# Optimization experiments

Measured on AMD Instinct MI355X. Metric: run time of the kernel, lower is better.

Reference implementation:

```python
import jax, jax.numpy as jnp
import numpy as np

N_NODES = 50000
N_EDGES = 800000
F_IN = 128
HEADS = 4
OUT_C = 32
NEG_SLOPE = 0.2


def setup_inputs() -> dict:
    key = jax.random.key(0)
    ks = jax.random.split(key, 6)
    x = jax.random.normal(ks[0], (N_NODES, F_IN), dtype=jnp.float32)
    edge_index = jax.random.randint(ks[1], (2, N_EDGES), 0, N_NODES, dtype=jnp.int32)
    scale = 1.0 / np.sqrt(F_IN)
    W_l = jax.random.normal(ks[2], (F_IN, HEADS * OUT_C), dtype=jnp.float32) * scale
    W_r = jax.random.normal(ks[3], (F_IN, HEADS * OUT_C), dtype=jnp.float32) * scale
    b_l = jnp.zeros((HEADS * OUT_C,), dtype=jnp.float32)
    b_r = jnp.zeros((HEADS * OUT_C,), dtype=jnp.float32)
    att = jax.random.normal(ks[4], (1, HEADS, OUT_C), dtype=jnp.float32) * (1.0 / np.sqrt(OUT_C))
    bias = jnp.zeros((HEADS * OUT_C,), dtype=jnp.float32)
    return {"x": x, "edge_index": edge_index, "W_l": W_l, "b_l": b_l,
            "W_r": W_r, "b_r": b_r, "att": att, "bias": bias}


def reference(x, edge_index, W_l, b_l, W_r, b_r, att, bias):
    N = x.shape[0]
    H, C = HEADS, OUT_C
    src, dst = edge_index[0], edge_index[1]  # messages flow src(j) -> dst(i)

    x_l = (x @ W_l + b_l).reshape(N, H, C)  # Theta_t x (source/message transform)
    x_r = (x @ W_r + b_r).reshape(N, H, C)  # Theta_s x (target transform)

    # per-edge GATv2 score: a^T LeakyReLU(x_l[j] + x_r[i])
    e = x_l[src] + x_r[dst]                        # [E, H, C]
    e = jnp.where(e > 0, e, NEG_SLOPE * e)         # LeakyReLU
    alpha = jnp.sum(e * att, axis=-1)              # [E, H]

    # segment softmax over incoming edges of each dst node
    amax = jax.ops.segment_max(alpha, dst, num_segments=N)   # [N, H]
    amax = jnp.where(jnp.isfinite(amax), amax, 0.0)
    expa = jnp.exp(alpha - amax[dst])                        # [E, H]
    denom = jax.ops.segment_sum(expa, dst, num_segments=N)   # [N, H]
    alpha = expa / (denom[dst] + 1e-16)                      # [E, H]

    # scatter-aggregate messages: sum_j alpha_ij * x_l[j]
    msg = alpha[:, :, None] * x_l[src]                       # [E, H, C]
    out = jax.ops.segment_sum(msg, dst, num_segments=N)      # [N, H, C]
    out = out.reshape(N, H * C) + bias                       # concat heads + bias
    return out
```

## Files before the change

kernel.cpp:

```cpp
#include <hip/hip_runtime.h>
#include <math.h>

#define NNODES 50000
#define NEDGES 800000
#define FIN 128
#define HC 128
#define NHEADS 4
#define NEG 0.2f
#define CAP 64
#define RANGE ((NNODES + 7) / 8)
#define GEMMB (((NNODES + 63) / 64) * 2)
#define HCHUNK ((NEDGES + 2047) / 2048)
#define HISTB (HCHUNK * 8)
#define ZB    ((NNODES + 255) / 256)
#define WTB   128

typedef _Float16 half8 __attribute__((ext_vector_type(8)));
typedef _Float16 half4v __attribute__((ext_vector_type(4)));
typedef float    f32x4 __attribute__((ext_vector_type(4)));

__global__ __launch_bounds__(256) void zero_wt_kernel(int* __restrict__ deg,
                                                      const float* __restrict__ Wl,
                                                      const float* __restrict__ Wr,
                                                      _Float16* __restrict__ Wt) {
    int t = threadIdx.x;
    if (blockIdx.x < ZB) {
        int i = blockIdx.x * 256 + t;
        if (i < NNODES) deg[i] = 0;
        return;
    }
    int flat = (blockIdx.x - ZB) * 256 + t;
    int k = flat >> 8, c = flat & 255;
    float v = (c < 128) ? Wl[(size_t)k * 128 + c] : Wr[(size_t)k * 128 + (c - 128)];
    Wt[(size_t)c * 128 + k] = (_Float16)v;
}

__global__ __launch_bounds__(256) void gemm_kernel(const float* __restrict__ x,
                                                   const _Float16* __restrict__ Wt,
                                                   const float* __restrict__ bl,
                                                   const float* __restrict__ br,
                                                   _Float16* __restrict__ xlh,
                                                   _Float16* __restrict__ xrh) {
    __shared__ _Float16 Asl[64 * 128];
    __shared__ _Float16 Bsl[128 * 128];
    int t = threadIdx.x;
    int nh = blockIdx.x & 1;
    int mb = blockIdx.x >> 1;

    {
        int row = t >> 2, q = t & 3;
        int node = mb * 64 + row;
        const float* xp = x + (size_t)(node < NNODES ? node : NNODES - 1) * FIN;
        float4 fa[8];
        #pragma unroll
        for (int uu = 0; uu < 4; ++uu) {
            fa[uu * 2]     = *(const float4*)(xp + (q * 4 + uu) * 8);
            fa[uu * 2 + 1] = *(const float4*)(xp + (q * 4 + uu) * 8 + 4);
        }
        #pragma unroll
        for (int uu = 0; uu < 4; ++uu) {
            int u = q * 4 + uu;
            float4 f0 = fa[uu * 2], f1 = fa[uu * 2 + 1];
            half8 h = { (_Float16)f0.x, (_Float16)f0.y, (_Float16)f0.z, (_Float16)f0.w,
                        (_Float16)f1.x, (_Float16)f1.y, (_Float16)f1.z, (_Float16)f1.w };
            *(half8*)&Asl[row * 128 + (u ^ (row & 7)) * 8] = h;
        }
        const _Float16* Wh = Wt + (size_t)nh * 128 * 128;
        half8 vb[8];
        #pragma unroll
        for (int i = 0; i < 8; ++i)
            vb[i] = *(const half8*)(Wh + (size_t)(t + i * 256) * 8);
        #pragma unroll
        for (int i = 0; i < 8; ++i) {
            int j = t + i * 256;
            int col = j >> 4, u = j & 15;
            *(half8*)&Bsl[col * 128 + (u ^ (col & 7)) * 8] = vb[i];
        }
    }
    __syncthreads();

    int wv = t >> 6, lane = t & 63;
    int ln15 = lane & 15, g = lane >> 4;
    const float* bb = nh ? br : bl;
    _Float16*    oo = nh ? xrh : xlh;

    float bias_v[8];
    #pragma unroll
    for (int nb = 0; nb < 8; ++nb)
        bias_v[nb] = bb[nb * 16 + ln15];

    half8 afrag[4];
    #pragma unroll
    for (int ks = 0; ks < 4; ++ks) {
        int rowa = wv * 16 + ln15;
        int ku = ks * 4 + g;
        afrag[ks] = *(half8*)&Asl[rowa * 128 + (ku ^ (rowa & 7)) * 8];
    }

    f32x4 acc[8];
    #pragma unroll
    for (int nb = 0; nb < 8; ++nb) acc[nb] = (f32x4){0.f, 0.f, 0.f, 0.f};

    #pragma unroll
    for (int ks = 0; ks < 4; ++ks) {
        int ku = ks * 4 + g;
        #pragma unroll
        for (int nb = 0; nb < 8; ++nb) {
            int col = nb * 16 + ln15;
            half8 bfrag = *(half8*)&Bsl[col * 128 + (ku ^ (col & 7)) * 8];
            acc[nb] = __builtin_amdgcn_mfma_f32_16x16x32_f16(afrag[ks], bfrag, acc[nb], 0, 0, 0);
        }
    }

    #pragma unroll
    for (int nb = 0; nb < 8; ++nb) {
        int cm = nb * 16 + ln15;
        #pragma unroll
        for (int i = 0; i < 4; ++i) {
            int node = mb * 64 + wv * 16 + g * 4 + i;
            if (node < NNODES)
                oo[(size_t)node * HC + cm] = (_Float16)(acc[nb][i] + bias_v[nb]);
        }
    }
}

__global__ __launch_bounds__(256) void hist_bucket_kernel(const int* __restrict__ src,
                                                          const int* __restrict__ dst,
                                                          int* __restrict__ deg,
                                                          unsigned short* __restrict__ bucket) {
    int r     = blockIdx.x & 7;
    int chunk = blockIdx.x >> 3;
    int rlo = r * RANGE, rhi = rlo + RANGE;
    int base = (chunk * 256 + threadIdx.x) * 8;

    #define COMMIT(d, s)                                                       \
    if ((d) >= rlo && (d) < rhi) {                                             \
        int p = atomicAdd(&deg[d], 1);                                         \
        if (p < CAP) bucket[(size_t)(d) * CAP + p] = (unsigned short)(s);      \
    }

    if (base + 7 < NEDGES) {
        int4 d0 = *(const int4*)(dst + base);
        int4 d1 = *(const int4*)(dst + base + 4);
        int4 s0 = *(const int4*)(src + base);
        int4 s1 = *(const int4*)(src + base + 4);
        COMMIT(d0.x, s0.x) COMMIT(d0.y, s0.y) COMMIT(d0.z, s0.z) COMMIT(d0.w, s0.w)
        COMMIT(d1.x, s1.x) COMMIT(d1.y, s1.y) COMMIT(d1.z, s1.z) COMMIT(d1.w, s1.w)
    } else {
        for (int i = base; i < NEDGES; ++i) {
            int dd = dst[i];
            COMMIT(dd, src[i])
        }
    }
    #undef COMMIT
}

__global__ __launch_bounds__(256) void fused_aggr_kernel(const int* __restrict__ deg,
                                                         const unsigned short* __restrict__ bucket,
                                                         const _Float16* __restrict__ xlh,
                                                         const _Float16* __restrict__ xrh,
                                                         const float* __restrict__ att,
                                                         const float* __restrict__ bias,
                                                         float* __restrict__ out) {
    int wid = threadIdx.x >> 6, lane = threadIdx.x & 63;
    int node = blockIdx.x * 4 + wid;
    if (node >= NNODES) return;
    int l32 = lane & 31, hl = lane >> 5;
    int c0 = l32 * 4;
    half4v xh = *(const half4v*)(xrh + (size_t)node * HC + c0);
    float4 xrv = make_float4((float)xh[0], (float)xh[1], (float)xh[2], (float)xh[3]);
    float4 atv = *(const float4*)(att + c0);
    float4 bv  = *(const float4*)(bias + c0);
    int dg = deg[node];
    dg = dg < CAP ? dg : CAP;
    int pbeg = node * CAP;
    int pend = pbeg + dg;
    float acc0 = 0.f, acc1 = 0.f, acc2 = 0.f, acc3 = 0.f, den = 0.f;

    #define EBODY(mh, valid)                                                   \
    {                                                                          \
        float m0 = (float)mh[0], m1 = (float)mh[1];                            \
        float m2 = (float)mh[2], m3 = (float)mh[3];                            \
        float a0 = m0 + xrv.x; a0 = a0 > 0.f ? a0 : NEG * a0;                  \
        float a1 = m1 + xrv.y; a1 = a1 > 0.f ? a1 : NEG * a1;                  \
        float a2 = m2 + xrv.z; a2 = a2 > 0.f ? a2 : NEG * a2;                  \
        float a3 = m3 + xrv.w; a3 = a3 > 0.f ? a3 : NEG * a3;                  \
        float pp = a0 * atv.x + a1 * atv.y + a2 * atv.z + a3 * atv.w;          \
        pp += __shfl_xor(pp, 1);                                               \
        pp += __shfl_xor(pp, 2);                                               \
        pp += __shfl_xor(pp, 4);                                               \
        float e = __expf(pp) * (valid);                                        \
        acc0 += e * m0; acc1 += e * m1; acc2 += e * m2; acc3 += e * m3;        \
        den += e;                                                              \
    }

    int p = pbeg;
    for (; p + 7 < pend; p += 8) {
        int s0 = bucket[p + hl],     s1 = bucket[p + 2 + hl];
        int s2 = bucket[p + 4 + hl], s3 = bucket[p + 6 + hl];
        half4v mh0 = *(const half4v*)(xlh + (size_t)s0 * HC + c0);
        half4v mh1 = *(const half4v*)(xlh + (size_t)s1 * HC + c0);
        half4v mh2 = *(const half4v*)(xlh + (size_t)s2 * HC + c0);
        half4v mh3 = *(const half4v*)(xlh + (size_t)s3 * HC + c0);
        EBODY(mh0, 1.f); EBODY(mh1, 1.f); EBODY(mh2, 1.f); EBODY(mh3, 1.f);
    }
    for (; p + 1 < pend; p += 2) {
        int s = bucket[p + hl];
        half4v mh = *(const half4v*)(xlh + (size_t)s * HC + c0);
        EBODY(mh, 1.f);
    }
    if (p < pend) {
        int s = bucket[p];
        half4v mh = *(const half4v*)(xlh + (size_t)s * HC + c0);
        EBODY(mh, hl ? 0.f : 1.f);
    }
    #undef EBODY

    acc0 += __shfl_xor(acc0, 32); acc1 += __shfl_xor(acc1, 32);
    acc2 += __shfl_xor(acc2, 32); acc3 += __shfl_xor(acc3, 32);
    den  += __shfl_xor(den, 32);

    if (hl == 0) {
        float inv = 1.0f / (den + 1e-16f);
        float4 o;
        o.x = acc0 * inv + bv.x;
        o.y = acc1 * inv + bv.y;
        o.z = acc2 * inv + bv.z;
        o.w = acc3 * inv + bv.w;
        *(float4*)(out + (size_t)node * HC + c0) = o;
    }
}

extern "C" void kernel_launch(void* const* d_in, const int* in_sizes, int n_in,
                              void* d_out, int out_size, void* d_ws, size_t ws_size,
                              hipStream_t stream) {
    const float* x    = (const float*)d_in[0];
    const int*   ei   = (const int*)  d_in[1];
    const float* Wl   = (const float*)d_in[2];
    const float* bl   = (const float*)d_in[3];
    const float* Wr   = (const float*)d_in[4];
    const float* br   = (const float*)d_in[5];
    const float* att  = (const float*)d_in[6];
    const float* bias = (const float*)d_in[7];
    float* out = (float*)d_out;

    _Float16* xlh = (_Float16*)d_ws;
    _Float16* xrh = xlh + (size_t)NNODES * HC;
    _Float16* Wt  = xrh + (size_t)NNODES * HC;
    int* deg = (int*)(Wt + 256 * 128);
    unsigned short* bucket = (unsigned short*)(deg + NNODES);

    const int* srcp = ei;
    const int* dstp = ei + NEDGES;

    zero_wt_kernel<<<ZB + WTB, 256, 0, stream>>>(deg, Wl, Wr, Wt);
    gemm_kernel<<<GEMMB, 256, 0, stream>>>(x, Wt, bl, br, xlh, xrh);
    hist_bucket_kernel<<<HISTB, 256, 0, stream>>>(srcp, dstp, deg, bucket);
    fused_aggr_kernel<<<(NNODES + 3) / 4, 256, 0, stream>>>(deg, bucket, xlh, xrh, att, bias, out);
}
```

Baseline: 111.1 us.

## Store projected features head-major and aggregate one head per wavefront

```diff
diff --git a/kernel.cpp b/kernel.cpp
--- a/kernel.cpp
+++ b/kernel.cpp
@@ -14,6 +14,7 @@
 #define HISTB (HCHUNK * 8)
 #define ZB    ((NNODES + 255) / 256)
 #define WTB   128
+#define AGGRB (((NNODES + 3) / 4) * 4)
 
 typedef _Float16 half8 __attribute__((ext_vector_type(8)));
 typedef _Float16 half4v __attribute__((ext_vector_type(4)));
@@ -114,12 +115,13 @@
 
     #pragma unroll
     for (int nb = 0; nb < 8; ++nb) {
-        int cm = nb * 16 + ln15;
+        size_t hbase = (size_t)(nb >> 1) * NNODES * 32;
+        int wc = (nb & 1) * 16 + ln15;
         #pragma unroll
         for (int i = 0; i < 4; ++i) {
             int node = mb * 64 + wv * 16 + g * 4 + i;
             if (node < NNODES)
-                oo[(size_t)node * HC + cm] = (_Float16)(acc[nb][i] + bias_v[nb]);
+                oo[hbase + (size_t)node * 32 + wc] = (_Float16)(acc[nb][i] + bias_v[nb]);
         }
     }
 }
@@ -163,71 +165,61 @@
                                                          const float* __restrict__ bias,
                                                          float* __restrict__ out) {
     int wid = threadIdx.x >> 6, lane = threadIdx.x & 63;
-    int node = blockIdx.x * 4 + wid;
+    int h    = blockIdx.x & 3;
+    int node = (blockIdx.x >> 2) * 4 + wid;
     if (node >= NNODES) return;
-    int l32 = lane & 31, hl = lane >> 5;
-    int c0 = l32 * 4;
-    half4v xh = *(const half4v*)(xrh + (size_t)node * HC + c0);
+    int g8 = lane >> 3;
+    int l8 = lane & 7;
+    const _Float16* xl_h = xlh + (size_t)h * NNODES * 32;
+    const _Float16* xr_h = xrh + (size_t)h * NNODES * 32;
+
+    half4v xh = *(const half4v*)(xr_h + (size_t)node * 32 + l8 * 4);
     float4 xrv = make_float4((float)xh[0], (float)xh[1], (float)xh[2], (float)xh[3]);
-    float4 atv = *(const float4*)(att + c0);
-    float4 bv  = *(const float4*)(bias + c0);
+    float4 atv = *(const float4*)(att + h * 32 + l8 * 4);
+
     int dg = deg[node];
     dg = dg < CAP ? dg : CAP;
     int pbeg = node * CAP;
-    int pend = pbeg + dg;
     float acc0 = 0.f, acc1 = 0.f, acc2 = 0.f, acc3 = 0.f, den = 0.f;
 
-    #define EBODY(mh, valid)                                                   \
-    {                                                                          \
-        float m0 = (float)mh[0], m1 = (float)mh[1];                            \
-        float m2 = (float)mh[2], m3 = (float)mh[3];                            \
-        float a0 = m0 + xrv.x; a0 = a0 > 0.f ? a0 : NEG * a0;                  \
-        float a1 = m1 + xrv.y; a1 = a1 > 0.f ? a1 : NEG * a1;                  \
-        float a2 = m2 + xrv.z; a2 = a2 > 0.f ? a2 : NEG * a2;                  \
-        float a3 = m3 + xrv.w; a3 = a3 > 0.f ? a3 : NEG * a3;                  \
-        float pp = a0 * atv.x + a1 * atv.y + a2 * atv.z + a3 * atv.w;          \
-        pp += __shfl_xor(pp, 1);                                               \
-        pp += __shfl_xor(pp, 2);                                               \
-        pp += __shfl_xor(pp, 4);                                               \
-        float e = __expf(pp) * (valid);                                        \
-        acc0 += e * m0; acc1 += e * m1; acc2 += e * m2; acc3 += e * m3;        \
-        den += e;                                                              \
-    }
-
-    int p = pbeg;
-    for (; p + 7 < pend; p += 8) {
-        int s0 = bucket[p + hl],     s1 = bucket[p + 2 + hl];
-        int s2 = bucket[p + 4 + hl], s3 = bucket[p + 6 + hl];
-        half4v mh0 = *(const half4v*)(xlh + (size_t)s0 * HC + c0);
-        half4v mh1 = *(const half4v*)(xlh + (size_t)s1 * HC + c0);
-        half4v mh2 = *(const half4v*)(xlh + (size_t)s2 * HC + c0);
-        half4v mh3 = *(const half4v*)(xlh + (size_t)s3 * HC + c0);
-        EBODY(mh0, 1.f); EBODY(mh1, 1.f); EBODY(mh2, 1.f); EBODY(mh3, 1.f);
-    }
-    for (; p + 1 < pend; p += 2) {
-        int s = bucket[p + hl];
-        half4v mh = *(const half4v*)(xlh + (size_t)s * HC + c0);
-        EBODY(mh, 1.f);
-    }
-    if (p < pend) {
-        int s = bucket[p];
-        half4v mh = *(const half4v*)(xlh + (size_t)s * HC + c0);
-        EBODY(mh, hl ? 0.f : 1.f);
-    }
-    #undef EBODY
-
-    acc0 += __shfl_xor(acc0, 32); acc1 += __shfl_xor(acc1, 32);
-    acc2 += __shfl_xor(acc2, 32); acc3 += __shfl_xor(acc3, 32);
-    den  += __shfl_xor(den, 32);
-
-    if (hl == 0) {
+    for (int it = 0; it < dg; it += 8) {
+        int idx = it + g8;
+        float valid = (idx < dg) ? 1.f : 0.f;
+        int s = bucket[pbeg + (idx < dg ? idx : 0)];
+        half4v mh = *(const half4v*)(xl_h + (size_t)s * 32 + l8 * 4);
+        float m0 = (float)mh[0], m1 = (float)mh[1];
+        float m2 = (float)mh[2], m3 = (float)mh[3];
+        float a0 = m0 + xrv.x; a0 = a0 > 0.f ? a0 : NEG * a0;
+        float a1 = m1 + xrv.y; a1 = a1 > 0.f ? a1 : NEG * a1;
+        float a2 = m2 + xrv.z; a2 = a2 > 0.f ? a2 : NEG * a2;
+        float a3 = m3 + xrv.w; a3 = a3 > 0.f ? a3 : NEG * a3;
+        float pp = a0 * atv.x + a1 * atv.y + a2 * atv.z + a3 * atv.w;
+        pp += __shfl_xor(pp, 1);
+        pp += __shfl_xor(pp, 2);
+        pp += __shfl_xor(pp, 4);
+        float e = __expf(pp) * valid;
+        acc0 += e * m0; acc1 += e * m1; acc2 += e * m2; acc3 += e * m3;
+        den += e;
+    }
+
+    #pragma unroll
+    for (int mask = 8; mask < 64; mask <<= 1) {
+        acc0 += __shfl_xor(acc0, mask);
+        acc1 += __shfl_xor(acc1, mask);
+        acc2 += __shfl_xor(acc2, mask);
+        acc3 += __shfl_xor(acc3, mask);
+        den  += __shfl_xor(den, mask);
+    }
+
+    if (g8 == 0) {
+        float4 bv = *(const float4*)(bias + h * 32 + l8 * 4);
         float inv = 1.0f / (den + 1e-16f);
         float4 o;
         o.x = acc0 * inv + bv.x;
         o.y = acc1 * inv + bv.y;
         o.z = acc2 * inv + bv.z;
         o.w = acc3 * inv + bv.w;
-        *(float4*)(out + (size_t)node * HC + c0) = o;
+        *(float4*)(out + (size_t)node * HC + h * 32 + l8 * 4) = o;
     }
 }
 
@@ -256,5 +248,5 @@
     zero_wt_kernel<<<ZB + WTB, 256, 0, stream>>>(deg, Wl, Wr, Wt);
     gemm_kernel<<<GEMMB, 256, 0, stream>>>(x, Wt, bl, br, xlh, xrh);
     hist_bucket_kernel<<<HISTB, 256, 0, stream>>>(srcp, dstp, deg, bucket);
-    fused_aggr_kernel<<<(NNODES + 3) / 4, 256, 0, stream>>>(deg, bucket, xlh, xrh, att, bias, out);
-}
+    fused_aggr_kernel<<<AGGRB, 256, 0, stream>>>(deg, bucket, xlh, xrh, att, bias, out);
+}
```

Measured after the change: 159.4 us. 1.43x slower.
